# Kernel tuning notes

Hardware: AMD Instinct MI355X
Metric: run time of the kernel (lower is better)

The kernel has to match this reference:

```python
import jax, jax.numpy as jnp
import numpy as np

N_NODES = 10000
N_EDGES = 640000
IN_C = 128
HID = 256
OUT_C = 256


def _linear_params(key, fan_in, fan_out):
    k1, k2 = jax.random.split(key)
    bound = 1.0 / np.sqrt(fan_in)
    W = jax.random.uniform(k1, (fan_in, fan_out), jnp.float32, -bound, bound)
    b = jax.random.uniform(k2, (fan_out,), jnp.float32, -bound, bound)
    return W, b


def setup_inputs() -> dict:
    key = jax.random.key(0)
    ks = jax.random.split(key, 8)
    x = jax.random.normal(ks[0], (N_NODES, IN_C), jnp.float32)
    edge_index = jax.random.randint(ks[1], (2, N_EDGES), 0, N_NODES, jnp.int32)
    W0a, b0a = _linear_params(ks[2], IN_C, HID)
    W0b, b0b = _linear_params(ks[3], HID, HID)
    W1a, b1a = _linear_params(ks[4], HID, HID)
    W1b, b1b = _linear_params(ks[5], HID, HID)
    W2a, b2a = _linear_params(ks[6], HID, OUT_C)
    W2b, b2b = _linear_params(ks[7], OUT_C, OUT_C)
    return {"x": x, "edge_index": edge_index,
            "W0a": W0a, "b0a": b0a, "W0b": W0b, "b0b": b0b,
            "W1a": W1a, "b1a": b1a, "W1b": W1b, "b1b": b1b,
            "W2a": W2a, "b2a": b2a, "W2b": W2b, "b2b": b2b}


def _gin_conv(x, src, dst, Wa, ba, Wb, bb):
    # sum-aggregate neighbor features: agg[i] = sum_{(j->i) in E} x[j]
    agg = jax.ops.segment_sum(x[src], dst, num_segments=N_NODES)
    h = x + agg  # eps = 0 (PyG GINConv default): (1+eps)*x + agg
    h = jnp.maximum(h @ Wa + ba, 0.0) @ Wb + bb  # Linear-ReLU-Linear MLP
    return h


def reference(x, edge_index, W0a, b0a, W0b, b0b, W1a, b1a, W1b, b1b, W2a, b2a, W2b, b2b):
    src, dst = edge_index[0], edge_index[1]
    h = _gin_conv(x, src, dst, W0a, b0a, W0b, b0b)
    h = jnp.maximum(h, 0.0)  # ReLU; dropout is identity in eval mode
    h = _gin_conv(h, src, dst, W1a, b1a, W1b, b1b)
    h = jnp.maximum(h, 0.0)
    h = _gin_conv(h, src, dst, W2a, b2a, W2b, b2b)
    return h
```

## Files before the change

kernel.cpp:

```cpp
#include <hip/hip_runtime.h>

#define N_NODES 10000
#define N_EDGES 640000
#define ELL_W   128

typedef short short8 __attribute__((ext_vector_type(8)));
typedef float f32x4 __attribute__((ext_vector_type(4)));

__device__ inline float bf2f(unsigned short u) {
    return __uint_as_float(((unsigned)u) << 16);
}
__device__ inline unsigned short f2bf(float f) {
    unsigned u = __float_as_uint(f);
    u += 0x7fffu + ((u >> 16) & 1u);
    return (unsigned short)(u >> 16);
}

__global__ __launch_bounds__(256) void fill_ell(const int* __restrict__ src,
                                                const int* __restrict__ dst,
                                                int* __restrict__ deg,
                                                unsigned short* __restrict__ ell) {
    int e = blockIdx.x * 256 + threadIdx.x;
    if (e >= N_EDGES) return;
    int d = dst[e];
    int pos = atomicAdd(&deg[d], 1);
    if (pos < ELL_W) ell[(size_t)d * ELL_W + pos] = (unsigned short)src[e];
}

__global__ __launch_bounds__(256) void cvt_x_kernel(const float4* __restrict__ x,
                                                    ushort4* __restrict__ xb, int n4) {
    int i = blockIdx.x * 256 + threadIdx.x;
    if (i >= n4) return;
    float4 v = x[i];
    ushort4 o;
    o.x = f2bf(v.x); o.y = f2bf(v.y); o.z = f2bf(v.z); o.w = f2bf(v.w);
    xb[i] = o;
}

struct WList {
    const float* src[6];
    unsigned short* dst[6];
    int K[6];
    int off[7];
};

__global__ __launch_bounds__(256) void cvt_w_kernel(WList wl, int total) {
    int idx = blockIdx.x * 256 + threadIdx.x;
    if (idx >= total) return;
    int w = 0;
    while (idx >= wl.off[w + 1]) ++w;
    int r = idx - wl.off[w];
    int k = r >> 8;
    int n = r & 255;
    wl.dst[w][(size_t)n * wl.K[w] + k] = f2bf(wl.src[w][r]);
}

template <int U2STRIDE>
__global__ __launch_bounds__(256) void gather_ell(const unsigned* __restrict__ x,
                                                  const unsigned short* __restrict__ ell,
                                                  const int* __restrict__ deg,
                                                  unsigned* __restrict__ out) {
    int wid = (blockIdx.x * 256 + threadIdx.x) >> 6;
    int lane = threadIdx.x & 63;
    if (wid >= N_NODES) return;
    int off = blockIdx.y * 64 + lane;

    unsigned v = x[(size_t)wid * U2STRIDE + off];
    float a0 = bf2f((unsigned short)(v & 0xffff));
    float a1 = bf2f((unsigned short)(v >> 16));

    int dg = min(deg[wid], ELL_W);
    const unsigned short* row = ell + (size_t)wid * ELL_W;

    int j = 0;
    for (; j + 8 <= dg; j += 8) {
        ushort4 sA = *(const ushort4*)(row + j);
        ushort4 sB = *(const ushort4*)(row + j + 4);
        unsigned v0 = x[(size_t)sA.x * U2STRIDE + off];
        unsigned v1 = x[(size_t)sA.y * U2STRIDE + off];
        unsigned v2 = x[(size_t)sA.z * U2STRIDE + off];
        unsigned v3 = x[(size_t)sA.w * U2STRIDE + off];
        unsigned v4 = x[(size_t)sB.x * U2STRIDE + off];
        unsigned v5 = x[(size_t)sB.y * U2STRIDE + off];
        unsigned v6 = x[(size_t)sB.z * U2STRIDE + off];
        unsigned v7 = x[(size_t)sB.w * U2STRIDE + off];
        a0 += (bf2f((unsigned short)(v0 & 0xffff)) + bf2f((unsigned short)(v1 & 0xffff))) +
              (bf2f((unsigned short)(v2 & 0xffff)) + bf2f((unsigned short)(v3 & 0xffff))) +
              (bf2f((unsigned short)(v4 & 0xffff)) + bf2f((unsigned short)(v5 & 0xffff))) +
              (bf2f((unsigned short)(v6 & 0xffff)) + bf2f((unsigned short)(v7 & 0xffff)));
        a1 += (bf2f((unsigned short)(v0 >> 16)) + bf2f((unsigned short)(v1 >> 16))) +
              (bf2f((unsigned short)(v2 >> 16)) + bf2f((unsigned short)(v3 >> 16))) +
              (bf2f((unsigned short)(v4 >> 16)) + bf2f((unsigned short)(v5 >> 16))) +
              (bf2f((unsigned short)(v6 >> 16)) + bf2f((unsigned short)(v7 >> 16)));
    }
    for (; j < dg; ++j) {
        unsigned vv = x[(size_t)row[j] * U2STRIDE + off];
        a0 += bf2f((unsigned short)(vv & 0xffff));
        a1 += bf2f((unsigned short)(vv >> 16));
    }
    unsigned o = (unsigned)f2bf(a0) | ((unsigned)f2bf(a1) << 16);
    out[(size_t)wid * U2STRIDE + off] = o;
}

template <int KSTEPS, bool RELU, bool F32OUT>
__global__ __launch_bounds__(64) void gemm_mfma(const unsigned short* __restrict__ A,
                                                const unsigned short* __restrict__ Wt,
                                                const float* __restrict__ bias,
                                                void* __restrict__ Cout) {
    constexpr int K = KSTEPS * 32;
    int bid = blockIdx.x;
    int rowtile = bid >> 2;
    int nq = bid & 3;
    int r0 = rowtile * 32;
    int lane = threadIdx.x;
    int lrow = lane & 15;
    int lkg = lane >> 4;

    const short8* Ap0 = (const short8*)(A + (size_t)(r0 + lrow) * K + lkg * 8);
    const short8* Ap1 = (const short8*)(A + (size_t)(r0 + 16 + lrow) * K + lkg * 8);
    int n0 = nq * 64;
    const short8* Bp = (const short8*)(Wt + (size_t)(n0 + lrow) * K + lkg * 8);
    f32x4 acc[2][4] = {};

#pragma unroll
    for (int ks = 0; ks < KSTEPS; ++ks) {
        short8 a0 = Ap0[ks * 4];
        short8 a1 = Ap1[ks * 4];
        short8 b0 = Bp[ks * 4 + 0 * 2 * K];
        short8 b1 = Bp[ks * 4 + 1 * 2 * K];
        short8 b2 = Bp[ks * 4 + 2 * 2 * K];
        short8 b3 = Bp[ks * 4 + 3 * 2 * K];
        acc[0][0] = __builtin_amdgcn_mfma_f32_16x16x32_bf16(a0, b0, acc[0][0], 0, 0, 0);
        acc[0][1] = __builtin_amdgcn_mfma_f32_16x16x32_bf16(a0, b1, acc[0][1], 0, 0, 0);
        acc[0][2] = __builtin_amdgcn_mfma_f32_16x16x32_bf16(a0, b2, acc[0][2], 0, 0, 0);
        acc[0][3] = __builtin_amdgcn_mfma_f32_16x16x32_bf16(a0, b3, acc[0][3], 0, 0, 0);
        acc[1][0] = __builtin_amdgcn_mfma_f32_16x16x32_bf16(a1, b0, acc[1][0], 0, 0, 0);
        acc[1][1] = __builtin_amdgcn_mfma_f32_16x16x32_bf16(a1, b1, acc[1][1], 0, 0, 0);
        acc[1][2] = __builtin_amdgcn_mfma_f32_16x16x32_bf16(a1, b2, acc[1][2], 0, 0, 0);
        acc[1][3] = __builtin_amdgcn_mfma_f32_16x16x32_bf16(a1, b3, acc[1][3], 0, 0, 0);
    }

#pragma unroll
    for (int rg = 0; rg < 2; ++rg) {
        int orow = r0 + rg * 16 + lkg * 4;
#pragma unroll
        for (int nt = 0; nt < 4; ++nt) {
            int c = n0 + nt * 16 + lrow;
            float bv = bias[c];
#pragma unroll
            for (int r = 0; r < 4; ++r) {
                int grow = orow + r;
                if (grow >= N_NODES) continue;
                float v = acc[rg][nt][r] + bv;
                if (RELU) v = fmaxf(v, 0.f);
                if (F32OUT)
                    ((float*)Cout)[(size_t)grow * 256 + c] = v;
                else
                    ((unsigned short*)Cout)[(size_t)grow * 256 + c] = f2bf(v);
            }
        }
    }
}

extern "C" void kernel_launch(void* const* d_in, const int* in_sizes, int n_in,
                              void* d_out, int out_size, void* d_ws, size_t ws_size,
                              hipStream_t stream) {
    const float* x   = (const float*)d_in[0];
    const int*   ei  = (const int*)d_in[1];
    const int*   src = ei;
    const int*   dst = ei + N_EDGES;
    const float* W0a = (const float*)d_in[2];
    const float* b0a = (const float*)d_in[3];
    const float* W0b = (const float*)d_in[4];
    const float* b0b = (const float*)d_in[5];
    const float* W1a = (const float*)d_in[6];
    const float* b1a = (const float*)d_in[7];
    const float* W1b = (const float*)d_in[8];
    const float* b1b = (const float*)d_in[9];
    const float* W2a = (const float*)d_in[10];
    const float* b2a = (const float*)d_in[11];
    const float* W2b = (const float*)d_in[12];
    const float* b2b = (const float*)d_in[13];

    char* ws = (char*)d_ws;
    size_t off = 0;
    auto alloc = [&](size_t bytes) {
        void* p = ws + off;
        off += (bytes + 255) & ~(size_t)255;
        return p;
    };
    unsigned short* xb   = (unsigned short*)alloc((size_t)N_NODES * 128 * 2);
    unsigned short* B0   = (unsigned short*)alloc((size_t)N_NODES * 256 * 2);
    unsigned short* B1   = (unsigned short*)alloc((size_t)N_NODES * 256 * 2);
    unsigned short* B2   = (unsigned short*)alloc((size_t)N_NODES * 256 * 2);
    unsigned short* Wt0a = (unsigned short*)alloc(256 * 128 * 2);
    unsigned short* Wt0b = (unsigned short*)alloc(256 * 256 * 2);
    unsigned short* Wt1a = (unsigned short*)alloc(256 * 256 * 2);
    unsigned short* Wt1b = (unsigned short*)alloc(256 * 256 * 2);
    unsigned short* Wt2a = (unsigned short*)alloc(256 * 256 * 2);
    unsigned short* Wt2b = (unsigned short*)alloc(256 * 256 * 2);
    int*            deg  = (int*)alloc(N_NODES * 4);
    unsigned short* ell  = (unsigned short*)alloc((size_t)N_NODES * ELL_W * 2);

    int edgeBlocks = (N_EDGES + 255) / 256;
    dim3 gatherGrid1((N_NODES + 3) / 4, 1);
    dim3 gatherGrid2((N_NODES + 3) / 4, 2);
    int gemmBlocks = ((N_NODES + 31) / 32) * 4;

    hipMemsetAsync(deg, 0, N_NODES * sizeof(int), stream);
    fill_ell<<<edgeBlocks, 256, 0, stream>>>(src, dst, deg, ell);

    cvt_x_kernel<<<(N_NODES * 128 / 4 + 255) / 256, 256, 0, stream>>>(
        (const float4*)x, (ushort4*)xb, N_NODES * 128 / 4);
    WList wl;
    wl.src[0] = W0a; wl.dst[0] = Wt0a; wl.K[0] = 128;
    wl.src[1] = W0b; wl.dst[1] = Wt0b; wl.K[1] = 256;
    wl.src[2] = W1a; wl.dst[2] = Wt1a; wl.K[2] = 256;
    wl.src[3] = W1b; wl.dst[3] = Wt1b; wl.K[3] = 256;
    wl.src[4] = W2a; wl.dst[4] = Wt2a; wl.K[4] = 256;
    wl.src[5] = W2b; wl.dst[5] = Wt2b; wl.K[5] = 256;
    int total = 0;
    for (int i = 0; i < 6; ++i) { wl.off[i] = total; total += wl.K[i] * 256; }
    wl.off[6] = total;
    cvt_w_kernel<<<(total + 255) / 256, 256, 0, stream>>>(wl, total);

    gather_ell<64><<<gatherGrid1, 256, 0, stream>>>((const unsigned*)xb, ell, deg, (unsigned*)B0);
    gemm_mfma<4, true, false><<<gemmBlocks, 64, 0, stream>>>(B0, Wt0a, b0a, B1);
    gemm_mfma<8, true, false><<<gemmBlocks, 64, 0, stream>>>(B1, Wt0b, b0b, B2);
    gather_ell<128><<<gatherGrid2, 256, 0, stream>>>((const unsigned*)B2, ell, deg, (unsigned*)B0);
    gemm_mfma<8, true, false><<<gemmBlocks, 64, 0, stream>>>(B0, Wt1a, b1a, B1);
    gemm_mfma<8, true, false><<<gemmBlocks, 64, 0, stream>>>(B1, Wt1b, b1b, B2);
    gather_ell<128><<<gatherGrid2, 256, 0, stream>>>((const unsigned*)B2, ell, deg, (unsigned*)B0);
    gemm_mfma<8, true, false><<<gemmBlocks, 64, 0, stream>>>(B0, Wt2a, b2a, B1);
    gemm_mfma<8, false, true><<<gemmBlocks, 64, 0, stream>>>(B1, Wt2b, b2b, d_out);
}
```

Baseline: 195.1 us.

## Fuse two-layer MLP via LDS, bucket edges for ELL build, split gathers

Merges each pair of Linear-ReLU-Linear GEMMs into one kernel that keeps the 32-row hidden tile in shared memory, so the hidden activation no longer round-trips through global memory. The atomic-per-edge ELL fill becomes a two-pass scheme: edges are first binned by 64-node bucket in shared memory, then each bucket builds its ELL rows locally and writes them out coalesced. Each 256-wide gather is split into two launches, one per column half, instead of a 2D grid. The fixed bucket capacities (LCAP, BCAP) silently drop edges if a chunk or bucket overflows, which holds for uniform random edges but not for arbitrary graphs.

New measurement: 202.5 us. +3.8%, slower.

```diff
diff --git a/kernel.cpp b/kernel.cpp
--- a/kernel.cpp
+++ b/kernel.cpp
@@ -3,6 +3,10 @@
 #define N_NODES 10000
 #define N_EDGES 640000
 #define ELL_W   128
+#define NB      157
+#define BCAP    4600
+#define LCAP    80
+#define CHUNK   2500
 
 typedef short short8 __attribute__((ext_vector_type(8)));
 typedef float f32x4 __attribute__((ext_vector_type(4)));
@@ -16,15 +20,76 @@
     return (unsigned short)(u >> 16);
 }
 
-__global__ __launch_bounds__(256) void fill_ell(const int* __restrict__ src,
-                                                const int* __restrict__ dst,
-                                                int* __restrict__ deg,
-                                                unsigned short* __restrict__ ell) {
-    int e = blockIdx.x * 256 + threadIdx.x;
-    if (e >= N_EDGES) return;
-    int d = dst[e];
-    int pos = atomicAdd(&deg[d], 1);
-    if (pos < ELL_W) ell[(size_t)d * ELL_W + pos] = (unsigned short)src[e];
+__global__ __launch_bounds__(256) void zero_cursor(int* __restrict__ g) {
+    if (threadIdx.x < NB) g[threadIdx.x] = 0;
+}
+
+__global__ __launch_bounds__(256) void bin_edges(const int* __restrict__ src,
+                                                 const int* __restrict__ dst,
+                                                 int* __restrict__ gCursor,
+                                                 unsigned* __restrict__ gBucket) {
+    __shared__ unsigned bins[NB][LCAP];
+    __shared__ int cnt[NB];
+    __shared__ int base[NB];
+    int t = threadIdx.x;
+    for (int i = t; i < NB; i += 256) cnt[i] = 0;
+    __syncthreads();
+
+    int e0 = blockIdx.x * CHUNK;
+    int e1 = min(e0 + CHUNK, N_EDGES);
+    for (int e = e0 + t; e < e1; e += 256) {
+        int d = dst[e];
+        int b = d >> 6;
+        unsigned pk = ((unsigned)src[e] << 6) | (unsigned)(d & 63);
+        int p = atomicAdd(&cnt[b], 1);
+        if (p < LCAP) bins[b][p] = pk;
+    }
+    __syncthreads();
+    for (int i = t; i < NB; i += 256) {
+        int c = min(cnt[i], LCAP);
+        cnt[i] = c;
+        base[i] = atomicAdd(&gCursor[i], c);
+    }
+    __syncthreads();
+    for (int b = 0; b < NB; ++b) {
+        int ba = base[b];
+        int n = min(cnt[b], max(0, BCAP - ba));
+        for (int i = t; i < n; i += 256)
+            gBucket[(size_t)b * BCAP + ba + i] = bins[b][i];
+    }
+}
+
+__global__ __launch_bounds__(256) void build_ell(const unsigned* __restrict__ gBucket,
+                                                 const int* __restrict__ gCursor,
+                                                 unsigned short* __restrict__ ell,
+                                                 int* __restrict__ deg) {
+    __shared__ unsigned short rows[64 * ELL_W];
+    __shared__ int ldeg[64];
+    int b = blockIdx.x;
+    int t = threadIdx.x;
+    for (int i = t; i < 64; i += 256) ldeg[i] = 0;
+    __syncthreads();
+
+    int n = min(gCursor[b], BCAP);
+    const unsigned* bk = gBucket + (size_t)b * BCAP;
+    for (int i = t; i < n; i += 256) {
+        unsigned pk = bk[i];
+        int local = pk & 63;
+        int s = pk >> 6;
+        int p = atomicAdd(&ldeg[local], 1);
+        if (p < ELL_W) rows[local * ELL_W + p] = (unsigned short)s;
+    }
+    __syncthreads();
+
+    int node0 = b * 64;
+    int nNodes = min(64, N_NODES - node0);
+    if (nNodes <= 0) return;
+    for (int i = t; i < nNodes; i += 256)
+        deg[node0 + i] = min(ldeg[i], ELL_W);
+    int totalVec = nNodes * (ELL_W / 8);
+    short8* dstv = (short8*)(ell + (size_t)node0 * ELL_W);
+    const short8* srcv = (const short8*)rows;
+    for (int i = t; i < totalVec; i += 256) dstv[i] = srcv[i];
 }
 
 __global__ __launch_bounds__(256) void cvt_x_kernel(const float4* __restrict__ x,
@@ -59,11 +124,11 @@
 __global__ __launch_bounds__(256) void gather_ell(const unsigned* __restrict__ x,
                                                   const unsigned short* __restrict__ ell,
                                                   const int* __restrict__ deg,
-                                                  unsigned* __restrict__ out) {
+                                                  unsigned* __restrict__ out, int half) {
     int wid = (blockIdx.x * 256 + threadIdx.x) >> 6;
     int lane = threadIdx.x & 63;
     if (wid >= N_NODES) return;
-    int off = blockIdx.y * 64 + lane;
+    int off = half * 64 + lane;
 
     unsigned v = x[(size_t)wid * U2STRIDE + off];
     float a0 = bf2f((unsigned short)(v & 0xffff));
@@ -102,61 +167,102 @@
     out[(size_t)wid * U2STRIDE + off] = o;
 }
 
-template <int KSTEPS, bool RELU, bool F32OUT>
-__global__ __launch_bounds__(64) void gemm_mfma(const unsigned short* __restrict__ A,
-                                                const unsigned short* __restrict__ Wt,
-                                                const float* __restrict__ bias,
+template <int KSTEPS, bool RELU2, bool F32OUT>
+__global__ __launch_bounds__(256) void mlp_mfma(const unsigned short* __restrict__ A,
+                                                const unsigned short* __restrict__ WtA,
+                                                const float* __restrict__ biasA,
+                                                const unsigned short* __restrict__ WtB,
+                                                const float* __restrict__ biasB,
                                                 void* __restrict__ Cout) {
-    constexpr int K = KSTEPS * 32;
-    int bid = blockIdx.x;
-    int rowtile = bid >> 2;
-    int nq = bid & 3;
-    int r0 = rowtile * 32;
-    int lane = threadIdx.x;
+    constexpr int K1 = KSTEPS * 32;
+    constexpr int LP = 264;
+    __shared__ unsigned short hid[32 * LP];
+
+    int r0 = blockIdx.x * 32;
+    int tid = threadIdx.x;
+    int lane = tid & 63;
+    int nq = tid >> 6;
     int lrow = lane & 15;
     int lkg = lane >> 4;
-
-    const short8* Ap0 = (const short8*)(A + (size_t)(r0 + lrow) * K + lkg * 8);
-    const short8* Ap1 = (const short8*)(A + (size_t)(r0 + 16 + lrow) * K + lkg * 8);
     int n0 = nq * 64;
-    const short8* Bp = (const short8*)(Wt + (size_t)(n0 + lrow) * K + lkg * 8);
-    f32x4 acc[2][4] = {};
-
-#pragma unroll
-    for (int ks = 0; ks < KSTEPS; ++ks) {
-        short8 a0 = Ap0[ks * 4];
-        short8 a1 = Ap1[ks * 4];
-        short8 b0 = Bp[ks * 4 + 0 * 2 * K];
-        short8 b1 = Bp[ks * 4 + 1 * 2 * K];
-        short8 b2 = Bp[ks * 4 + 2 * 2 * K];
-        short8 b3 = Bp[ks * 4 + 3 * 2 * K];
-        acc[0][0] = __builtin_amdgcn_mfma_f32_16x16x32_bf16(a0, b0, acc[0][0], 0, 0, 0);
-        acc[0][1] = __builtin_amdgcn_mfma_f32_16x16x32_bf16(a0, b1, acc[0][1], 0, 0, 0);
-        acc[0][2] = __builtin_amdgcn_mfma_f32_16x16x32_bf16(a0, b2, acc[0][2], 0, 0, 0);
-        acc[0][3] = __builtin_amdgcn_mfma_f32_16x16x32_bf16(a0, b3, acc[0][3], 0, 0, 0);
-        acc[1][0] = __builtin_amdgcn_mfma_f32_16x16x32_bf16(a1, b0, acc[1][0], 0, 0, 0);
-        acc[1][1] = __builtin_amdgcn_mfma_f32_16x16x32_bf16(a1, b1, acc[1][1], 0, 0, 0);
-        acc[1][2] = __builtin_amdgcn_mfma_f32_16x16x32_bf16(a1, b2, acc[1][2], 0, 0, 0);
-        acc[1][3] = __builtin_amdgcn_mfma_f32_16x16x32_bf16(a1, b3, acc[1][3], 0, 0, 0);
-    }
-
-#pragma unroll
-    for (int rg = 0; rg < 2; ++rg) {
-        int orow = r0 + rg * 16 + lkg * 4;
-#pragma unroll
-        for (int nt = 0; nt < 4; ++nt) {
-            int c = n0 + nt * 16 + lrow;
-            float bv = bias[c];
-#pragma unroll
-            for (int r = 0; r < 4; ++r) {
-                int grow = orow + r;
-                if (grow >= N_NODES) continue;
-                float v = acc[rg][nt][r] + bv;
-                if (RELU) v = fmaxf(v, 0.f);
-                if (F32OUT)
-                    ((float*)Cout)[(size_t)grow * 256 + c] = v;
-                else
-                    ((unsigned short*)Cout)[(size_t)grow * 256 + c] = f2bf(v);
+
+    {
+        const short8* Ap0 = (const short8*)(A + (size_t)(r0 + lrow) * K1 + lkg * 8);
+        const short8* Ap1 = (const short8*)(A + (size_t)(r0 + 16 + lrow) * K1 + lkg * 8);
+        const short8* Bp = (const short8*)(WtA + (size_t)(n0 + lrow) * K1 + lkg * 8);
+        f32x4 acc[2][4] = {};
+#pragma unroll
+        for (int ks = 0; ks < KSTEPS; ++ks) {
+            short8 a0 = Ap0[ks * 4];
+            short8 a1 = Ap1[ks * 4];
+            short8 b0 = Bp[ks * 4 + 0 * 2 * K1];
+            short8 b1 = Bp[ks * 4 + 1 * 2 * K1];
+            short8 b2 = Bp[ks * 4 + 2 * 2 * K1];
+            short8 b3 = Bp[ks * 4 + 3 * 2 * K1];
+            acc[0][0] = __builtin_amdgcn_mfma_f32_16x16x32_bf16(a0, b0, acc[0][0], 0, 0, 0);
+            acc[0][1] = __builtin_amdgcn_mfma_f32_16x16x32_bf16(a0, b1, acc[0][1], 0, 0, 0);
+            acc[0][2] = __builtin_amdgcn_mfma_f32_16x16x32_bf16(a0, b2, acc[0][2], 0, 0, 0);
+            acc[0][3] = __builtin_amdgcn_mfma_f32_16x16x32_bf16(a0, b3, acc[0][3], 0, 0, 0);
+            acc[1][0] = __builtin_amdgcn_mfma_f32_16x16x32_bf16(a1, b0, acc[1][0], 0, 0, 0);
+            acc[1][1] = __builtin_amdgcn_mfma_f32_16x16x32_bf16(a1, b1, acc[1][1], 0, 0, 0);
+            acc[1][2] = __builtin_amdgcn_mfma_f32_16x16x32_bf16(a1, b2, acc[1][2], 0, 0, 0);
+            acc[1][3] = __builtin_amdgcn_mfma_f32_16x16x32_bf16(a1, b3, acc[1][3], 0, 0, 0);
+        }
+#pragma unroll
+        for (int rg = 0; rg < 2; ++rg) {
+            int row = rg * 16 + lkg * 4;
+#pragma unroll
+            for (int nt = 0; nt < 4; ++nt) {
+                int c = n0 + nt * 16 + lrow;
+                float bv = biasA[c];
+#pragma unroll
+                for (int r = 0; r < 4; ++r) {
+                    float v = fmaxf(acc[rg][nt][r] + bv, 0.f);
+                    hid[(row + r) * LP + c] = f2bf(v);
+                }
+            }
+        }
+    }
+    __syncthreads();
+
+    {
+        const short8* Bp = (const short8*)(WtB + (size_t)(n0 + lrow) * 256 + lkg * 8);
+        f32x4 acc[2][4] = {};
+#pragma unroll
+        for (int ks = 0; ks < 8; ++ks) {
+            short8 a0 = *(const short8*)&hid[lrow * LP + ks * 32 + lkg * 8];
+            short8 a1 = *(const short8*)&hid[(16 + lrow) * LP + ks * 32 + lkg * 8];
+            short8 b0 = Bp[ks * 4 + 0 * 2 * 256];
+            short8 b1 = Bp[ks * 4 + 1 * 2 * 256];
+            short8 b2 = Bp[ks * 4 + 2 * 2 * 256];
+            short8 b3 = Bp[ks * 4 + 3 * 2 * 256];
+            acc[0][0] = __builtin_amdgcn_mfma_f32_16x16x32_bf16(a0, b0, acc[0][0], 0, 0, 0);
+            acc[0][1] = __builtin_amdgcn_mfma_f32_16x16x32_bf16(a0, b1, acc[0][1], 0, 0, 0);
+            acc[0][2] = __builtin_amdgcn_mfma_f32_16x16x32_bf16(a0, b2, acc[0][2], 0, 0, 0);
+            acc[0][3] = __builtin_amdgcn_mfma_f32_16x16x32_bf16(a0, b3, acc[0][3], 0, 0, 0);
+            acc[1][0] = __builtin_amdgcn_mfma_f32_16x16x32_bf16(a1, b0, acc[1][0], 0, 0, 0);
+            acc[1][1] = __builtin_amdgcn_mfma_f32_16x16x32_bf16(a1, b1, acc[1][1], 0, 0, 0);
+            acc[1][2] = __builtin_amdgcn_mfma_f32_16x16x32_bf16(a1, b2, acc[1][2], 0, 0, 0);
+            acc[1][3] = __builtin_amdgcn_mfma_f32_16x16x32_bf16(a1, b3, acc[1][3], 0, 0, 0);
+        }
+#pragma unroll
+        for (int rg = 0; rg < 2; ++rg) {
+            int orow = r0 + rg * 16 + lkg * 4;
+#pragma unroll
+            for (int nt = 0; nt < 4; ++nt) {
+                int c = n0 + nt * 16 + lrow;
+                float bv = biasB[c];
+#pragma unroll
+                for (int r = 0; r < 4; ++r) {
+                    int grow = orow + r;
+                    if (grow >= N_NODES) continue;
+                    float v = acc[rg][nt][r] + bv;
+                    if (RELU2) v = fmaxf(v, 0.f);
+                    if (F32OUT)
+                        ((float*)Cout)[(size_t)grow * 256 + c] = v;
+                    else
+                        ((unsigned short*)Cout)[(size_t)grow * 256 + c] = f2bf(v);
+                }
             }
         }
     }
@@ -189,26 +295,26 @@
         off += (bytes + 255) & ~(size_t)255;
         return p;
     };
-    unsigned short* xb   = (unsigned short*)alloc((size_t)N_NODES * 128 * 2);
-    unsigned short* B0   = (unsigned short*)alloc((size_t)N_NODES * 256 * 2);
-    unsigned short* B1   = (unsigned short*)alloc((size_t)N_NODES * 256 * 2);
-    unsigned short* B2   = (unsigned short*)alloc((size_t)N_NODES * 256 * 2);
-    unsigned short* Wt0a = (unsigned short*)alloc(256 * 128 * 2);
-    unsigned short* Wt0b = (unsigned short*)alloc(256 * 256 * 2);
-    unsigned short* Wt1a = (unsigned short*)alloc(256 * 256 * 2);
-    unsigned short* Wt1b = (unsigned short*)alloc(256 * 256 * 2);
-    unsigned short* Wt2a = (unsigned short*)alloc(256 * 256 * 2);
-    unsigned short* Wt2b = (unsigned short*)alloc(256 * 256 * 2);
-    int*            deg  = (int*)alloc(N_NODES * 4);
-    unsigned short* ell  = (unsigned short*)alloc((size_t)N_NODES * ELL_W * 2);
-
-    int edgeBlocks = (N_EDGES + 255) / 256;
-    dim3 gatherGrid1((N_NODES + 3) / 4, 1);
-    dim3 gatherGrid2((N_NODES + 3) / 4, 2);
-    int gemmBlocks = ((N_NODES + 31) / 32) * 4;
-
-    hipMemsetAsync(deg, 0, N_NODES * sizeof(int), stream);
-    fill_ell<<<edgeBlocks, 256, 0, stream>>>(src, dst, deg, ell);
+    unsigned short* xb    = (unsigned short*)alloc((size_t)N_NODES * 128 * 2);
+    unsigned short* B0    = (unsigned short*)alloc((size_t)N_NODES * 256 * 2);
+    unsigned short* B2    = (unsigned short*)alloc((size_t)N_NODES * 256 * 2);
+    unsigned short* Wt0a  = (unsigned short*)alloc(256 * 128 * 2);
+    unsigned short* Wt0b  = (unsigned short*)alloc(256 * 256 * 2);
+    unsigned short* Wt1a  = (unsigned short*)alloc(256 * 256 * 2);
+    unsigned short* Wt1b  = (unsigned short*)alloc(256 * 256 * 2);
+    unsigned short* Wt2a  = (unsigned short*)alloc(256 * 256 * 2);
+    unsigned short* Wt2b  = (unsigned short*)alloc(256 * 256 * 2);
+    int*            deg   = (int*)alloc(N_NODES * 4);
+    unsigned short* ell   = (unsigned short*)alloc((size_t)N_NODES * ELL_W * 2);
+    int*            gCur  = (int*)alloc(NB * 4);
+    unsigned*       gBkt  = (unsigned*)alloc((size_t)NB * BCAP * 4);
+
+    int gatherBlocks = (N_NODES + 3) / 4;
+    int mlpBlocks = (N_NODES + 31) / 32;
+
+    zero_cursor<<<1, 256, 0, stream>>>(gCur);
+    bin_edges<<<(N_EDGES + CHUNK - 1) / CHUNK, 256, 0, stream>>>(src, dst, gCur, gBkt);
+    build_ell<<<NB, 256, 0, stream>>>(gBkt, gCur, ell, deg);
 
     cvt_x_kernel<<<(N_NODES * 128 / 4 + 255) / 256, 256, 0, stream>>>(
         (const float4*)x, (ushort4*)xb, N_NODES * 128 / 4);
@@ -224,13 +330,12 @@
     wl.off[6] = total;
     cvt_w_kernel<<<(total + 255) / 256, 256, 0, stream>>>(wl, total);
 
-    gather_ell<64><<<gatherGrid1, 256, 0, stream>>>((const unsigned*)xb, ell, deg, (unsigned*)B0);
-    gemm_mfma<4, true, false><<<gemmBlocks, 64, 0, stream>>>(B0, Wt0a, b0a, B1);
-    gemm_mfma<8, true, false><<<gemmBlocks, 64, 0, stream>>>(B1, Wt0b, b0b, B2);
-    gather_ell<128><<<gatherGrid2, 256, 0, stream>>>((const unsigned*)B2, ell, deg, (unsigned*)B0);
-    gemm_mfma<8, true, false><<<gemmBlocks, 64, 0, stream>>>(B0, Wt1a, b1a, B1);
-    gemm_mfma<8, true, false><<<gemmBlocks, 64, 0, stream>>>(B1, Wt1b, b1b, B2);
-    gather_ell<128><<<gatherGrid2, 256, 0, stream>>>((const unsigned*)B2, ell, deg, (unsigned*)B0);
-    gemm_mfma<8, true, false><<<gemmBlocks, 64, 0, stream>>>(B0, Wt2a, b2a, B1);
-    gemm_mfma<8, false, true><<<gemmBlocks, 64, 0, stream>>>(B1, Wt2b, b2b, d_out);
-}
+    gather_ell<64><<<gatherBlocks, 256, 0, stream>>>((const unsigned*)xb, ell, deg, (unsigned*)B0, 0);
+    mlp_mfma<4, true, false><<<mlpBlocks, 256, 0, stream>>>(B0, Wt0a, b0a, Wt0b, b0b, B2);
+    gather_ell<128><<<gatherBlocks, 256, 0, stream>>>((const unsigned*)B2, ell, deg, (unsigned*)B0, 0);
+    gather_ell<128><<<gatherBlocks, 256, 0, stream>>>((const unsigned*)B2, ell, deg, (unsigned*)B0, 1);
+    mlp_mfma<8, true, false><<<mlpBlocks, 256, 0, stream>>>(B0, Wt1a, b1a, Wt1b, b1b, B2);
+    gather_ell<128><<<gatherBlocks, 256, 0, stream>>>((const unsigned*)B2, ell, deg, (unsigned*)B0, 0);
+    gather_ell<128><<<gatherBlocks, 256, 0, stream>>>((const unsigned*)B2, ell, deg, (unsigned*)B0, 1);
+    mlp_mfma<8, false, true><<<mlpBlocks, 256, 0, stream>>>(B0, Wt2a, b2a, Wt2b, b2b, d_out);
+}
```

## Build ELL adjacency via two-pass shared-memory binning instead of global atomics

Applied to the files above, without the earlier changes.

Replaces the per-edge global atomicAdd scatter into the ELL table with a two-stage build. Edges are first binned by destination block of 64 nodes in shared memory, then flushed to global buckets. Per-bucket blocks then assemble the ELL rows in LDS and write them out with coalesced vector stores. This cuts contended global atomics and scattered 2-byte writes, at the cost of an extra kernel pass and fixed bucket capacities (LCAP, BCAP) that can silently drop edges when the degree distribution is skewed.

Measured after the change: 179.2 us. -8.1%, faster.

```diff
diff --git a/kernel.cpp b/kernel.cpp
--- a/kernel.cpp
+++ b/kernel.cpp
@@ -3,6 +3,10 @@
 #define N_NODES 10000
 #define N_EDGES 640000
 #define ELL_W   128
+#define NB      157
+#define BCAP    4600
+#define LCAP    80
+#define CHUNK   2500
 
 typedef short short8 __attribute__((ext_vector_type(8)));
 typedef float f32x4 __attribute__((ext_vector_type(4)));
@@ -16,15 +20,77 @@
     return (unsigned short)(u >> 16);
 }
 
-__global__ __launch_bounds__(256) void fill_ell(const int* __restrict__ src,
-                                                const int* __restrict__ dst,
-                                                int* __restrict__ deg,
-                                                unsigned short* __restrict__ ell) {
-    int e = blockIdx.x * 256 + threadIdx.x;
-    if (e >= N_EDGES) return;
-    int d = dst[e];
-    int pos = atomicAdd(&deg[d], 1);
-    if (pos < ELL_W) ell[(size_t)d * ELL_W + pos] = (unsigned short)src[e];
+__global__ __launch_bounds__(256) void zero_cursor(int* __restrict__ g) {
+    if (threadIdx.x < NB) g[threadIdx.x] = 0;
+}
+
+__global__ __launch_bounds__(256) void bin_edges(const int* __restrict__ src,
+                                                 const int* __restrict__ dst,
+                                                 int* __restrict__ gCursor,
+                                                 unsigned* __restrict__ gBucket) {
+    __shared__ unsigned bins[NB][LCAP];
+    __shared__ int cnt[NB];
+    __shared__ int base[NB];
+    int t = threadIdx.x;
+    for (int i = t; i < NB; i += 256) cnt[i] = 0;
+    __syncthreads();
+
+    int e0 = blockIdx.x * CHUNK;
+    int e1 = min(e0 + CHUNK, N_EDGES);
+    for (int e = e0 + t; e < e1; e += 256) {
+        int d = dst[e];
+        int b = d >> 6;
+        unsigned pk = ((unsigned)src[e] << 6) | (unsigned)(d & 63);
+        int p = atomicAdd(&cnt[b], 1);
+        if (p < LCAP) bins[b][p] = pk;
+    }
+    __syncthreads();
+    for (int i = t; i < NB; i += 256) {
+        int c = min(cnt[i], LCAP);
+        cnt[i] = c;
+        base[i] = atomicAdd(&gCursor[i], c);
+    }
+    __syncthreads();
+    int wave = t >> 6, lane = t & 63;
+    for (int b = wave; b < NB; b += 4) {
+        int ba = base[b];
+        int n = min(cnt[b], max(0, BCAP - ba));
+        for (int i = lane; i < n; i += 64)
+            gBucket[(size_t)b * BCAP + ba + i] = bins[b][i];
+    }
+}
+
+__global__ __launch_bounds__(256) void build_ell(const unsigned* __restrict__ gBucket,
+                                                 const int* __restrict__ gCursor,
+                                                 unsigned short* __restrict__ ell,
+                                                 int* __restrict__ deg) {
+    __shared__ unsigned short rows[64 * ELL_W];
+    __shared__ int ldeg[64];
+    int b = blockIdx.x;
+    int t = threadIdx.x;
+    for (int i = t; i < 64; i += 256) ldeg[i] = 0;
+    __syncthreads();
+
+    int n = min(gCursor[b], BCAP);
+    const unsigned* bk = gBucket + (size_t)b * BCAP;
+    for (int i = t; i < n; i += 256) {
+        unsigned pk = bk[i];
+        int local = pk & 63;
+        int s = pk >> 6;
+        int p = atomicAdd(&ldeg[local], 1);
+        if (p < ELL_W) rows[local * ELL_W + p] = (unsigned short)s;
+    }
+    __syncthreads();
+
+    int node0 = b * 64;
+    int nNodes = min(64, N_NODES - node0);
+    if (nNodes <= 0) return;
+    for (int i = t; i < nNodes; i += 256)
+        deg[node0 + i] = min(ldeg[i], ELL_W);
+    int totalVec = nNodes * (ELL_W / 8);
+    short8* dstv = (short8*)(ell + (size_t)node0 * ELL_W);
+    const short8* srcv = (const short8*)rows;
+    for (int i = t; i < totalVec; i += 256) dstv[i] = srcv[i];
 }
 
 __global__ __launch_bounds__(256) void cvt_x_kernel(const float4* __restrict__ x,
@@ -189,26 +255,28 @@
         off += (bytes + 255) & ~(size_t)255;
         return p;
     };
-    unsigned short* xb   = (unsigned short*)alloc((size_t)N_NODES * 128 * 2);
-    unsigned short* B0   = (unsigned short*)alloc((size_t)N_NODES * 256 * 2);
-    unsigned short* B1   = (unsigned short*)alloc((size_t)N_NODES * 256 * 2);
-    unsigned short* B2   = (unsigned short*)alloc((size_t)N_NODES * 256 * 2);
-    unsigned short* Wt0a = (unsigned short*)alloc(256 * 128 * 2);
-    unsigned short* Wt0b = (unsigned short*)alloc(256 * 256 * 2);
-    unsigned short* Wt1a = (unsigned short*)alloc(256 * 256 * 2);
-    unsigned short* Wt1b = (unsigned short*)alloc(256 * 256 * 2);
-    unsigned short* Wt2a = (unsigned short*)alloc(256 * 256 * 2);
-    unsigned short* Wt2b = (unsigned short*)alloc(256 * 256 * 2);
-    int*            deg  = (int*)alloc(N_NODES * 4);
-    unsigned short* ell  = (unsigned short*)alloc((size_t)N_NODES * ELL_W * 2);
-
-    int edgeBlocks = (N_EDGES + 255) / 256;
+    unsigned short* xb    = (unsigned short*)alloc((size_t)N_NODES * 128 * 2);
+    unsigned short* B0    = (unsigned short*)alloc((size_t)N_NODES * 256 * 2);
+    unsigned short* B1    = (unsigned short*)alloc((size_t)N_NODES * 256 * 2);
+    unsigned short* B2    = (unsigned short*)alloc((size_t)N_NODES * 256 * 2);
+    unsigned short* Wt0a  = (unsigned short*)alloc(256 * 128 * 2);
+    unsigned short* Wt0b  = (unsigned short*)alloc(256 * 256 * 2);
+    unsigned short* Wt1a  = (unsigned short*)alloc(256 * 256 * 2);
+    unsigned short* Wt1b  = (unsigned short*)alloc(256 * 256 * 2);
+    unsigned short* Wt2a  = (unsigned short*)alloc(256 * 256 * 2);
+    unsigned short* Wt2b  = (unsigned short*)alloc(256 * 256 * 2);
+    int*            deg   = (int*)alloc(N_NODES * 4);
+    unsigned short* ell   = (unsigned short*)alloc((size_t)N_NODES * ELL_W * 2);
+    int*            gCur  = (int*)alloc(NB * 4);
+    unsigned*       gBkt  = (unsigned*)alloc((size_t)NB * BCAP * 4);
+
     dim3 gatherGrid1((N_NODES + 3) / 4, 1);
     dim3 gatherGrid2((N_NODES + 3) / 4, 2);
     int gemmBlocks = ((N_NODES + 31) / 32) * 4;
 
-    hipMemsetAsync(deg, 0, N_NODES * sizeof(int), stream);
-    fill_ell<<<edgeBlocks, 256, 0, stream>>>(src, dst, deg, ell);
+    zero_cursor<<<1, 256, 0, stream>>>(gCur);
+    bin_edges<<<(N_EDGES + CHUNK - 1) / CHUNK, 256, 0, stream>>>(src, dst, gCur, gBkt);
+    build_ell<<<NB, 256, 0, stream>>>(gBkt, gCur, ell, deg);
 
     cvt_x_kernel<<<(N_NODES * 128 / 4 + 255) / 256, 256, 0, stream>>>(
         (const float4*)x, (ushort4*)xb, N_NODES * 128 / 4);
```
